# Optimization experiments

Hardware: AMD Instinct MI355X
Metric: run time of the kernel (lower is better)

The kernel has to match this reference:

```python
import jax, jax.numpy as jnp
import numpy as np

N, E, H, C, G = 100000, 400000, 4, 64, 64  # nodes, edges, heads, per-head dim, graphs
NEG_SLOPE = 0.2


def gat_conv(x, src, dst, W, a_src, a_dst, b, num_nodes):
    # PyG GATConv (v1), concat=True, eval mode (no dropout).
    h = (x @ W).reshape(num_nodes, H, C)                      # [N,H,C]
    al_src = (h * a_src).sum(-1)                              # [N,H]
    al_dst = (h * a_dst).sum(-1)                              # [N,H]
    e = jax.nn.leaky_relu(al_src[src] + al_dst[dst], NEG_SLOPE)  # [E',H]
    # segment softmax over incoming edges of each destination node
    m = jax.ops.segment_max(e, dst, num_segments=num_nodes)
    m = jnp.where(jnp.isfinite(m), m, 0.0)
    ex = jnp.exp(e - m[dst])
    s = jax.ops.segment_sum(ex, dst, num_segments=num_nodes)
    alpha = ex / (s[dst] + 1e-16)                             # [E',H]
    msg = h[src] * alpha[..., None]                           # [E',H,C]
    out = jax.ops.segment_sum(msg, dst, num_segments=num_nodes)
    return out.reshape(num_nodes, H * C) + b


def setup_inputs() -> dict:
    key = jax.random.key(0)
    ks = jax.random.split(key, 20)
    p = lambda k, shape: (jax.random.normal(k, shape, dtype=jnp.float32) * 0.05)
    inp = {
        "x": jax.random.normal(ks[0], (N, 2), dtype=jnp.float32),
        "edge_index": jax.random.randint(ks[1], (2, E), 0, N, dtype=jnp.int64),
        "batch": jnp.sort(jax.random.randint(ks[2], (N,), 0, G, dtype=jnp.int64)),
        # layer 1: in=2 -> heads*hidden=256
        "W1": p(ks[3], (2, H * C)), "a1s": p(ks[4], (H, C)), "a1d": p(ks[5], (H, C)), "b1": jnp.zeros((H * C,), jnp.float32),
        # layer 2,3: 256 -> 256
        "W2": p(ks[6], (H * C, H * C)), "a2s": p(ks[7], (H, C)), "a2d": p(ks[8], (H, C)), "b2": jnp.zeros((H * C,), jnp.float32),
        "W3": p(ks[9], (H * C, H * C)), "a3s": p(ks[10], (H, C)), "a3d": p(ks[11], (H, C)), "b3": jnp.zeros((H * C,), jnp.float32),
        # projection MLP 256 -> 512 -> 256
        "Wp1": p(ks[12], (H * C, 512)), "bp1": jnp.zeros((512,), jnp.float32),
        "Wp2": p(ks[13], (512, 256)), "bp2": jnp.zeros((256,), jnp.float32),
    }
    return inp


def reference(x, edge_index, batch, W1, a1s, a1d, b1, W2, a2s, a2d, b2,
              W3, a3s, a3d, b3, Wp1, bp1, Wp2, bp2):
    num_nodes = x.shape[0]
    # add_self_loops=True (PyG GATConv default); same edge set for all layers
    loops = jnp.arange(num_nodes, dtype=edge_index.dtype)
    src = jnp.concatenate([edge_index[0], loops])
    dst = jnp.concatenate([edge_index[1], loops])

    h = jax.nn.elu(gat_conv(x, src, dst, W1, a1s, a1d, b1, num_nodes))
    h = jax.nn.elu(gat_conv(h, src, dst, W2, a2s, a2d, b2, num_nodes))
    h = jax.nn.elu(gat_conv(h, src, dst, W3, a3s, a3d, b3, num_nodes))

    # global_mean_pool over graphs
    sums = jax.ops.segment_sum(h, batch, num_segments=G)            # [G,256]
    cnts = jax.ops.segment_sum(jnp.ones((num_nodes,), h.dtype), batch, num_segments=G)
    pooled = sums / jnp.maximum(cnts, 1.0)[:, None]

    # projection MLP (dropout is identity in eval)
    z = jax.nn.relu(pooled @ Wp1 + bp1)
    return z @ Wp2 + bp2
```

## Files before the change

kernel.cpp:

```cpp
#include <hip/hip_runtime.h>
#include <math.h>

#define HC 256
#define NHEAD 4
#define NEG_SLOPE 0.2f
#define GG 64

typedef unsigned short u16;
typedef unsigned int u32;
typedef __attribute__((ext_vector_type(8))) short short8;
typedef __attribute__((ext_vector_type(4))) float f32x4;

static __device__ inline u16 f2bf_rn(float f) {
  u32 x = __float_as_uint(f);
  u32 r = (x + 0x7fffu + ((x >> 16) & 1u)) >> 16;
  return (u16)r;
}
static __device__ inline float bf2f(u16 u) { return __uint_as_float(((u32)u) << 16); }


__global__ void count_deg_kernel(const int* __restrict__ ei, int E, int Nn, int* __restrict__ deg) {
  int idx = blockIdx.x * 256 + threadIdx.x;
  int Et = E + Nn;
  if (idx >= Et) return;
  int d = (idx < E) ? ei[E + idx] : (idx - E);
  atomicAdd(&deg[d], 1);
}

__global__ void scan_partial_kernel(const int* __restrict__ deg, int Nn,
                                    int* __restrict__ rowptr, int* __restrict__ bsum) {
  __shared__ int s[256];
  int t = threadIdx.x, i = blockIdx.x * 256 + t;
  int v = (i < Nn) ? deg[i] : 0;
  s[t] = v; __syncthreads();
  for (int off = 1; off < 256; off <<= 1) {
    int x = (t >= off) ? s[t - off] : 0; __syncthreads();
    s[t] += x; __syncthreads();
  }
  if (i < Nn) rowptr[i] = s[t] - v;
  if (t == 255) bsum[blockIdx.x] = s[t];
}

__global__ void scan_bsum_kernel(int* __restrict__ bsum, int nb) {
  __shared__ int s[512];
  int t = threadIdx.x;
  int v = (t < nb) ? bsum[t] : 0;
  s[t] = v; __syncthreads();
  for (int off = 1; off < 512; off <<= 1) {
    int x = (t >= off) ? s[t - off] : 0; __syncthreads();
    s[t] += x; __syncthreads();
  }
  if (t < nb) bsum[t] = s[t] - v;
}

__global__ void scan_add_kernel(int* __restrict__ rowptr, const int* __restrict__ bsum,
                                int Nn, int Etot) {
  int i = blockIdx.x * 256 + threadIdx.x;
  if (i < Nn) rowptr[i] += bsum[blockIdx.x];
  if (i == 0) rowptr[Nn] = Etot;
}

__global__ void fill_csr_kernel(const int* __restrict__ ei, int E, int Nn,
                                const int* __restrict__ rowptr, int* __restrict__ cursor,
                                int* __restrict__ col) {
  int idx = blockIdx.x * 256 + threadIdx.x;
  int Et = E + Nn;
  if (idx >= Et) return;
  int s, d;
  if (idx < E) { s = ei[idx]; d = ei[E + idx]; } else { s = d = idx - E; }
  int pos = atomicAdd(&cursor[d], 1);
  col[rowptr[d] + pos] = s;
}


__global__ void convert_w_kernel(const float* __restrict__ W, u16* __restrict__ hi) {
  int idx = blockIdx.x * 256 + threadIdx.x;
  if (idx >= 256 * 256) return;
  int k = idx >> 8, n = idx & 255;
  hi[n * 256 + k] = f2bf_rn(W[idx]);
}


__global__ void prep_va_kernel(const float* __restrict__ W1, const float* __restrict__ a1s,
                               const float* __restrict__ a1d, float* __restrict__ va) {
  int t = threadIdx.x;
  int q = t >> 6, lane = t & 63;
  int c = t;
  float asv = a1s[c], adv = a1d[c];
  float w0 = W1[c], w1 = W1[256 + c];
  float s0 = w0 * asv, s1 = w1 * asv, d0 = w0 * adv, d1 = w1 * adv;
  #pragma unroll
  for (int off = 32; off >= 1; off >>= 1) {
    s0 += __shfl_xor(s0, off, 64); s1 += __shfl_xor(s1, off, 64);
    d0 += __shfl_xor(d0, off, 64); d1 += __shfl_xor(d1, off, 64);
  }
  if (lane == 0) {
    va[q] = s0; va[4 + q] = s1;
    va[8 + q] = d0; va[12 + q] = d1;
  }
}

__global__ void logits1_kernel(const float* __restrict__ x, const float* __restrict__ va,
                               float* __restrict__ als, float* __restrict__ ald, int Nn) {
  int node = blockIdx.x * 256 + threadIdx.x;
  if (node >= Nn) return;
  float2 xv = *(const float2*)&x[(size_t)node * 2];
  float4 vs0 = *(const float4*)&va[0], vs1 = *(const float4*)&va[4];
  float4 vd0 = *(const float4*)&va[8], vd1 = *(const float4*)&va[12];
  float4 s, d;
  s.x = xv.x * vs0.x + xv.y * vs1.x; s.y = xv.x * vs0.y + xv.y * vs1.y;
  s.z = xv.x * vs0.z + xv.y * vs1.z; s.w = xv.x * vs0.w + xv.y * vs1.w;
  d.x = xv.x * vd0.x + xv.y * vd1.x; d.y = xv.x * vd0.y + xv.y * vd1.y;
  d.z = xv.x * vd0.z + xv.y * vd1.z; d.w = xv.x * vd0.w + xv.y * vd1.w;
  *(float4*)&als[node * 4] = s;
  *(float4*)&ald[node * 4] = d;
}

__global__ void sm_gather1_kernel(const float* __restrict__ x,
    const float* __restrict__ als, const float* __restrict__ ald,
    const int* __restrict__ rowptr, const int* __restrict__ col,
    float* __restrict__ xbar, int Nn) {
  int node = blockIdx.x * 256 + threadIdx.x;
  if (node >= Nn) return;
  int rs = rowptr[node], re = rowptr[node + 1];
  float4 ad = *(const float4*)&ald[node * 4];
  float S0 = 0.f, S1 = 0.f, S2 = 0.f, S3 = 0.f;
  float a0 = 0.f, a1 = 0.f, a2 = 0.f, a3 = 0.f, a4 = 0.f, a5 = 0.f, a6 = 0.f, a7 = 0.f;
  for (int i = rs; i < re; ++i) {
    int s = col[i];
    float4 a = *(const float4*)&als[(size_t)s * 4];
    float2 xs = *(const float2*)&x[(size_t)s * 2];
    float e0 = a.x + ad.x; e0 = e0 > 0.f ? e0 : NEG_SLOPE * e0;
    float e1 = a.y + ad.y; e1 = e1 > 0.f ? e1 : NEG_SLOPE * e1;
    float e2 = a.z + ad.z; e2 = e2 > 0.f ? e2 : NEG_SLOPE * e2;
    float e3 = a.w + ad.w; e3 = e3 > 0.f ? e3 : NEG_SLOPE * e3;
    float p0 = __expf(e0), p1 = __expf(e1), p2 = __expf(e2), p3 = __expf(e3);
    S0 += p0; S1 += p1; S2 += p2; S3 += p3;
    a0 += p0 * xs.x; a1 += p0 * xs.y;
    a2 += p1 * xs.x; a3 += p1 * xs.y;
    a4 += p2 * xs.x; a5 += p2 * xs.y;
    a6 += p3 * xs.x; a7 += p3 * xs.y;
  }
  float i0 = 1.f / (S0 + 1e-16f), i1 = 1.f / (S1 + 1e-16f);
  float i2 = 1.f / (S2 + 1e-16f), i3 = 1.f / (S3 + 1e-16f);
  *(float4*)&xbar[(size_t)node * 8]     = make_float4(a0 * i0, a1 * i0, a2 * i1, a3 * i1);
  *(float4*)&xbar[(size_t)node * 8 + 4] = make_float4(a4 * i2, a5 * i2, a6 * i3, a7 * i3);
}

__global__ __launch_bounds__(256) void expand1_kernel(const float* __restrict__ xbar,
    const float* __restrict__ W1, const float* __restrict__ b1,
    u16* __restrict__ out16, int Nn) {
  int node = blockIdx.x * 4 + (threadIdx.x >> 6);
  int lane = threadIdx.x & 63;
  if (node >= Nn) return;
  int hA = lane >> 5;
  float4 xb0 = *(const float4*)&xbar[(size_t)node * 8];
  float4 xb1 = *(const float4*)&xbar[(size_t)node * 8 + 4];
  float xA0 = hA ? xb0.z : xb0.x, xA1 = hA ? xb0.w : xb0.y;
  float xB0 = hA ? xb1.z : xb1.x, xB1 = hA ? xb1.w : xb1.y;
  int cA = 2 * lane, cB = 128 + 2 * lane;
  float2 wA0 = *(const float2*)&W1[cA], wA1 = *(const float2*)&W1[256 + cA];
  float2 wB0 = *(const float2*)&W1[cB], wB1 = *(const float2*)&W1[256 + cB];
  float2 bA = *(const float2*)&b1[cA],  bB = *(const float2*)&b1[cB];
  float o0 = xA0 * wA0.x + xA1 * wA1.x + bA.x;
  float o1 = xA0 * wA0.y + xA1 * wA1.y + bA.y;
  float o2 = xB0 * wB0.x + xB1 * wB1.x + bB.x;
  float o3 = xB0 * wB0.y + xB1 * wB1.y + bB.y;
  o0 = o0 > 0.f ? o0 : (__expf(o0) - 1.0f);
  o1 = o1 > 0.f ? o1 : (__expf(o1) - 1.0f);
  o2 = o2 > 0.f ? o2 : (__expf(o2) - 1.0f);
  o3 = o3 > 0.f ? o3 : (__expf(o3) - 1.0f);
  u32* o32 = (u32*)out16;
  o32[(size_t)node * 128 + lane]      = (u32)f2bf_rn(o0) | ((u32)f2bf_rn(o1) << 16);
  o32[(size_t)node * 128 + 64 + lane] = (u32)f2bf_rn(o2) | ((u32)f2bf_rn(o3) << 16);
}


#define GBM 64
#define GBN 128

__global__ __launch_bounds__(256) void gemm_mfma_kernel(
    const u16* __restrict__ A, const u16* __restrict__ Bt,
    const float* __restrict__ as_, const float* __restrict__ ad_,
    u16* __restrict__ C16, float* __restrict__ als, float* __restrict__ ald, int Mrows) {
  __shared__ __align__(16) u16 smem[24576];
  char* base_ = (char*)smem;
  int bc = blockIdx.x, br = blockIdx.y;
  int tid = threadIdx.x;
  int wid = tid >> 6, lane = tid & 63;
  int wr = wid >> 1, wc = wid & 1;
  int row0 = br * GBM, col0 = bc * GBN;
  int fr = lane & 15, fg = lane >> 4;

  const u16* agp[2];
  int wofA[2];
  #pragma unroll
  for (int p = 0; p < 2; ++p) {
    int row = p * 32 + (tid >> 3), c = tid & 7;
    int gr = row0 + row; if (gr >= Mrows) gr = Mrows - 1;
    agp[p] = A + (size_t)gr * 256 + c * 8;
    wofA[p] = row * 128 + ((c ^ (row & 7)) << 4);
  }
  const u16* bgp[4];
  int wofB[4];
  #pragma unroll
  for (int p = 0; p < 4; ++p) {
    int row = p * 32 + (tid >> 3), c = tid & 7;
    bgp[p] = Bt + (size_t)(col0 + row) * 256 + c * 8;
    wofB[p] = row * 128 + ((c ^ (row & 7)) << 4);
  }
  int rofA[2][2], rofB[2][4];
  #pragma unroll
  for (int ks = 0; ks < 2; ++ks) {
    #pragma unroll
    for (int m = 0; m < 2; ++m) {
      int rl = wr * 32 + m * 16 + fr;
      rofA[ks][m] = rl * 128 + (((ks * 4 + fg) ^ (rl & 7)) << 4);
    }
    #pragma unroll
    for (int n = 0; n < 4; ++n) {
      int cl_ = wc * 64 + n * 16 + fr;
      rofB[ks][n] = cl_ * 128 + (((ks * 4 + fg) ^ (cl_ & 7)) << 4);
    }
  }

  f32x4 acc[2][4];
  #pragma unroll
  for (int m = 0; m < 2; ++m)
    #pragma unroll
    for (int n = 0; n < 4; ++n) acc[m][n] = (f32x4){0.f, 0.f, 0.f, 0.f};

  uint4 va[2], vb[4];
  #pragma unroll
  for (int p = 0; p < 2; ++p) va[p] = *(const uint4*)agp[p];
  #pragma unroll
  for (int p = 0; p < 4; ++p) vb[p] = *(const uint4*)bgp[p];
  #pragma unroll
  for (int p = 0; p < 2; ++p) *(uint4*)(base_ + wofA[p]) = va[p];
  #pragma unroll
  for (int p = 0; p < 4; ++p) *(uint4*)(base_ + 16384 + wofB[p]) = vb[p];
  __syncthreads();

  #pragma unroll
  for (int kt = 0; kt < 4; ++kt) {
    int buf = kt & 1;
    if (kt < 3) {
      #pragma unroll
      for (int p = 0; p < 2; ++p) va[p] = *(const uint4*)(agp[p] + (kt + 1) * 64);
      #pragma unroll
      for (int p = 0; p < 4; ++p) vb[p] = *(const uint4*)(bgp[p] + (kt + 1) * 64);
    }
    #pragma unroll
    for (int ks = 0; ks < 2; ++ks) {
      short8 af[2], bf[4];
      #pragma unroll
      for (int m = 0; m < 2; ++m) af[m] = *(const short8*)(base_ + buf * 8192 + rofA[ks][m]);
      #pragma unroll
      for (int n = 0; n < 4; ++n) bf[n] = *(const short8*)(base_ + 16384 + buf * 16384 + rofB[ks][n]);
      #pragma unroll
      for (int m = 0; m < 2; ++m)
        #pragma unroll
        for (int n = 0; n < 4; ++n)
          acc[m][n] = __builtin_amdgcn_mfma_f32_16x16x32_bf16(af[m], bf[n], acc[m][n], 0, 0, 0);
    }
    if (kt < 3) {
      int nb = buf ^ 1;
      #pragma unroll
      for (int p = 0; p < 2; ++p) *(uint4*)(base_ + nb * 8192 + wofA[p]) = va[p];
      #pragma unroll
      for (int p = 0; p < 4; ++p) *(uint4*)(base_ + 16384 + nb * 16384 + wofB[p]) = vb[p];
      __syncthreads();
    }
  }

  u16* cl = smem;
  __syncthreads();
  #pragma unroll
  for (int m = 0; m < 2; ++m) {
    #pragma unroll
    for (int n = 0; n < 4; ++n) {
      int c = wc * 64 + n * 16 + fr;
      #pragma unroll
      for (int j = 0; j < 4; ++j) {
        int lr = wr * 32 + m * 16 + fg * 4 + j;
        cl[lr * 128 + c] = f2bf_rn(acc[m][n][j]);
      }
    }
  }
  __syncthreads();
  #pragma unroll
  for (int i = 0; i < 4; ++i) {
    int u = i * 256 + tid;
    int lr = u >> 4, ch = u & 15;
    int grow = row0 + lr;
    if (grow < Mrows) {
      uint4 v = *(const uint4*)&cl[lr * 128 + ch * 8];
      *(uint4*)&C16[(size_t)grow * 256 + col0 + ch * 8] = v;
    }
  }

  int head = bc * 2 + wc;
  float asv[4], adv[4];
  #pragma unroll
  for (int n = 0; n < 4; ++n) {
    asv[n] = as_[head * 64 + n * 16 + fr];
    adv[n] = ad_[head * 64 + n * 16 + fr];
  }
  #pragma unroll
  for (int m = 0; m < 2; ++m) {
    #pragma unroll
    for (int j = 0; j < 4; ++j) {
      float ps = 0.f, pd = 0.f;
      #pragma unroll
      for (int n = 0; n < 4; ++n) {
        ps += acc[m][n][j] * asv[n];
        pd += acc[m][n][j] * adv[n];
      }
      #pragma unroll
      for (int off = 1; off < 16; off <<= 1) {
        ps += __shfl_xor(ps, off, 64);
        pd += __shfl_xor(pd, off, 64);
      }
      int grow = row0 + wr * 32 + m * 16 + fg * 4 + j;
      if (fr == 0 && grow < Mrows) {
        als[grow * 4 + head] = ps;
        ald[grow * 4 + head] = pd;
      }
    }
  }
}


__global__ __launch_bounds__(256) void gat_gather_kernel(const u16* __restrict__ h16,
    const float* __restrict__ als, const float* __restrict__ ald,
    const int* __restrict__ rowptr, const int* __restrict__ col,
    const float* __restrict__ bias, u16* __restrict__ out16, int Nn) {
  int node = __builtin_amdgcn_readfirstlane(blockIdx.x * 4 + (threadIdx.x >> 6));
  int lane = threadIdx.x & 63;
  if (node >= Nn) return;
  int rs = rowptr[node], re = rowptr[node + 1];
  int head = lane >> 4;
  float adv = ald[(size_t)node * 4 + head];
  float S = 0.f;
  float a0 = 0.f, a1 = 0.f, a2 = 0.f, a3 = 0.f;
  const uint2* h64 = (const uint2*)h16;
  #pragma unroll 2
  for (int i = rs; i < re; ++i) {
    int s = col[i];
    float e = als[(size_t)s * 4 + head] + adv;
    e = e > 0.f ? e : NEG_SLOPE * e;
    float p = __expf(e);
    S += p;
    uint2 pv = h64[(size_t)s * 64 + lane];
    a0 += p * __uint_as_float(pv.x << 16);
    a1 += p * __uint_as_float(pv.x & 0xffff0000u);
    a2 += p * __uint_as_float(pv.y << 16);
    a3 += p * __uint_as_float(pv.y & 0xffff0000u);
  }
  float iS = 1.f / (S + 1e-16f);
  float4 bv = *(const float4*)&bias[4 * lane];
  float o0 = a0 * iS + bv.x;
  float o1 = a1 * iS + bv.y;
  float o2 = a2 * iS + bv.z;
  float o3 = a3 * iS + bv.w;
  o0 = o0 > 0.f ? o0 : (__expf(o0) - 1.0f);
  o1 = o1 > 0.f ? o1 : (__expf(o1) - 1.0f);
  o2 = o2 > 0.f ? o2 : (__expf(o2) - 1.0f);
  o3 = o3 > 0.f ? o3 : (__expf(o3) - 1.0f);
  uint2 ov;
  ov.x = (u32)f2bf_rn(o0) | ((u32)f2bf_rn(o1) << 16);
  ov.y = (u32)f2bf_rn(o2) | ((u32)f2bf_rn(o3) << 16);
  ((uint2*)out16)[(size_t)node * 64 + lane] = ov;
}


__global__ void bounds_kernel(const int* __restrict__ batch, int Nn, int* __restrict__ bounds) {
  int g = threadIdx.x;
  if (g > GG) return;
  int lo = 0, hi = Nn;
  while (lo < hi) { int mid = (lo + hi) >> 1; if (batch[mid] < g) lo = mid + 1; else hi = mid; }
  bounds[g] = lo;
}

__global__ __launch_bounds__(64) void pool_kernel(const u16* __restrict__ X,
    const int* __restrict__ bounds, float* __restrict__ pooled) {
  int g = blockIdx.x, split = blockIdx.y;
  int lane = threadIdx.x;
  int s = bounds[g], e = bounds[g + 1];
  int cnt = e - s;
  if (cnt <= 0) return;
  int chunk = (cnt + gridDim.y - 1) / gridDim.y;
  int s2 = s + split * chunk, e2 = min(e, s2 + chunk);
  if (s2 >= e2) return;
  int r = lane >> 5, c = lane & 31;
  float acc[8] = {};
  for (int n = s2 + r; n < e2; n += 2) {
    uint4 v = *(const uint4*)&X[(size_t)n * HC + c * 8];
    acc[0] += __uint_as_float(v.x << 16);
    acc[1] += __uint_as_float(v.x & 0xffff0000u);
    acc[2] += __uint_as_float(v.y << 16);
    acc[3] += __uint_as_float(v.y & 0xffff0000u);
    acc[4] += __uint_as_float(v.z << 16);
    acc[5] += __uint_as_float(v.z & 0xffff0000u);
    acc[6] += __uint_as_float(v.w << 16);
    acc[7] += __uint_as_float(v.w & 0xffff0000u);
  }
  #pragma unroll
  for (int j = 0; j < 8; ++j) acc[j] += __shfl_xor(acc[j], 32, 64);
  if (r == 0) {
    #pragma unroll
    for (int j = 0; j < 8; ++j) atomicAdd(&pooled[g * HC + c * 8 + j], acc[j]);
  }
}

__global__ __launch_bounds__(512) void mlp_kernel(const float* __restrict__ pooled,
    const int* __restrict__ bounds, const float* __restrict__ Wp1, const float* __restrict__ bp1,
    const float* __restrict__ Wp2, const float* __restrict__ bp2, float* __restrict__ out) {
  __shared__ float p[256];
  __shared__ float z1[512];
  int g = blockIdx.x, t = threadIdx.x;
  if (t < 256) {
    int cnt = bounds[g + 1] - bounds[g];
    float inv = 1.0f / (float)(cnt > 1 ? cnt : 1);
    p[t] = pooled[g * 256 + t] * inv;
  }
  __syncthreads();
  float a1 = bp1[t];
  for (int k = 0; k < 256; ++k) a1 += p[k] * Wp1[k * 512 + t];
  z1[t] = fmaxf(a1, 0.f);
  __syncthreads();
  if (t < 256) {
    float a2 = bp2[t];
    for (int k = 0; k < 512; ++k) a2 += z1[k] * Wp2[k * 256 + t];
    out[g * 256 + t] = a2;
  }
}


static inline size_t align_up(size_t x, size_t a) { return (x + a - 1) & ~(a - 1); }

extern "C" void kernel_launch(void* const* d_in, const int* in_sizes, int n_in,
                              void* d_out, int out_size, void* d_ws, size_t ws_size,
                              hipStream_t stream) {
  const float* x    = (const float*)d_in[0];
  const int*   ei   = (const int*)d_in[1];
  const int*   batch= (const int*)d_in[2];
  const float* W1   = (const float*)d_in[3];
  const float* a1s  = (const float*)d_in[4];
  const float* a1d  = (const float*)d_in[5];
  const float* b1   = (const float*)d_in[6];
  const float* W2   = (const float*)d_in[7];
  const float* a2s  = (const float*)d_in[8];
  const float* a2d  = (const float*)d_in[9];
  const float* b2   = (const float*)d_in[10];
  const float* W3   = (const float*)d_in[11];
  const float* a3s  = (const float*)d_in[12];
  const float* a3d  = (const float*)d_in[13];
  const float* b3   = (const float*)d_in[14];
  const float* Wp1  = (const float*)d_in[15];
  const float* bp1  = (const float*)d_in[16];
  const float* Wp2  = (const float*)d_in[17];
  const float* bp2  = (const float*)d_in[18];

  const int N = in_sizes[0] / 2;
  const int E = in_sizes[1] / 2;
  const int Et = E + N;

  char* base = (char*)d_ws;
  size_t off = 0;
  auto alloc = [&](size_t bytes) { size_t o = off; off = align_up(off + bytes, 256); return o; };
  u16*   h16    = (u16*)  (base + alloc((size_t)N * HC * 2));
  u16*   xhi    = (u16*)  (base + alloc((size_t)N * HC * 2));
  float* als    = (float*)(base + alloc((size_t)N * 4 * 4));
  float* ald    = (float*)(base + alloc((size_t)N * 4 * 4));
  float* xbar   = (float*)(base + alloc((size_t)N * 8 * 4));
  float* vabuf  = (float*)(base + alloc(16 * 4));
  int*   rowptr = (int*)  (base + alloc((size_t)(N + 1) * 4));
  int*   col    = (int*)  (base + alloc((size_t)Et * 4));
  int*   deg    = (int*)  (base + alloc((size_t)N * 4));
  int*   cursor = (int*)  (base + alloc((size_t)N * 4));
  int*   bsum   = (int*)  (base + alloc(512 * 4));
  int*   bounds = (int*)  (base + alloc((GG + 1) * 4));
  float* pooled = (float*)(base + alloc((size_t)GG * HC * 4));
  (void)ws_size; (void)n_in; (void)out_size;

  u16* W2t = (u16*)deg;
  u16* W3t = (u16*)cursor;

  hipMemsetAsync(deg, 0, (size_t)N * 4, stream);
  hipMemsetAsync(cursor, 0, (size_t)N * 4, stream);
  hipMemsetAsync(pooled, 0, (size_t)GG * HC * 4, stream);

  int ebk = (Et + 255) / 256;
  count_deg_kernel<<<ebk, 256, 0, stream>>>(ei, E, N, deg);
  int NT = (N + 255) / 256;
  scan_partial_kernel<<<NT, 256, 0, stream>>>(deg, N, rowptr, bsum);
  scan_bsum_kernel<<<1, 512, 0, stream>>>(bsum, NT);
  scan_add_kernel<<<NT, 256, 0, stream>>>(rowptr, bsum, N, Et);
  fill_csr_kernel<<<ebk, 256, 0, stream>>>(ei, E, N, rowptr, cursor, col);

  convert_w_kernel<<<256, 256, 0, stream>>>(W2, W2t);
  convert_w_kernel<<<256, 256, 0, stream>>>(W3, W3t);

  dim3 gemm_grid(HC / GBN, (N + GBM - 1) / GBM);
  int nodeblk = (N + 3) / 4;

  prep_va_kernel<<<1, 256, 0, stream>>>(W1, a1s, a1d, vabuf);
  logits1_kernel<<<NT, 256, 0, stream>>>(x, vabuf, als, ald, N);
  sm_gather1_kernel<<<NT, 256, 0, stream>>>(x, als, ald, rowptr, col, xbar, N);
  expand1_kernel<<<nodeblk, 256, 0, stream>>>(xbar, W1, b1, xhi, N);
  gemm_mfma_kernel<<<gemm_grid, 256, 0, stream>>>(xhi, W2t, a2s, a2d, h16, als, ald, N);
  gat_gather_kernel<<<nodeblk, 256, 0, stream>>>(h16, als, ald, rowptr, col, b2, xhi, N);
  gemm_mfma_kernel<<<gemm_grid, 256, 0, stream>>>(xhi, W3t, a3s, a3d, h16, als, ald, N);
  gat_gather_kernel<<<nodeblk, 256, 0, stream>>>(h16, als, ald, rowptr, col, b3, xhi, N);

  bounds_kernel<<<1, 128, 0, stream>>>(batch, N, bounds);
  pool_kernel<<<dim3(GG, 32), 64, 0, stream>>>(xhi, bounds, pooled);
  mlp_kernel<<<GG, 512, 0, stream>>>(pooled, bounds, Wp1, bp1, Wp2, bp2, (float*)d_out);
}
```

Measured before the change: 339.8 us.

## Fuse layer-1 logits into gather, merge prep kernels and memsets

```diff
diff --git a/kernel.cpp b/kernel.cpp
--- a/kernel.cpp
+++ b/kernel.cpp
@@ -73,67 +73,63 @@
 }
 
 
-__global__ void convert_w_kernel(const float* __restrict__ W, u16* __restrict__ hi) {
-  int idx = blockIdx.x * 256 + threadIdx.x;
-  if (idx >= 256 * 256) return;
-  int k = idx >> 8, n = idx & 255;
-  hi[n * 256 + k] = f2bf_rn(W[idx]);
-}
-
-
-__global__ void prep_va_kernel(const float* __restrict__ W1, const float* __restrict__ a1s,
-                               const float* __restrict__ a1d, float* __restrict__ va) {
-  int t = threadIdx.x;
-  int q = t >> 6, lane = t & 63;
-  int c = t;
-  float asv = a1s[c], adv = a1d[c];
-  float w0 = W1[c], w1 = W1[256 + c];
-  float s0 = w0 * asv, s1 = w1 * asv, d0 = w0 * adv, d1 = w1 * adv;
-  #pragma unroll
-  for (int off = 32; off >= 1; off >>= 1) {
-    s0 += __shfl_xor(s0, off, 64); s1 += __shfl_xor(s1, off, 64);
-    d0 += __shfl_xor(d0, off, 64); d1 += __shfl_xor(d1, off, 64);
-  }
-  if (lane == 0) {
-    va[q] = s0; va[4 + q] = s1;
-    va[8 + q] = d0; va[12 + q] = d1;
-  }
-}
-
-__global__ void logits1_kernel(const float* __restrict__ x, const float* __restrict__ va,
-                               float* __restrict__ als, float* __restrict__ ald, int Nn) {
-  int node = blockIdx.x * 256 + threadIdx.x;
+__global__ void prep_misc_kernel(const float* __restrict__ W2, const float* __restrict__ W3,
+                                 u16* __restrict__ W2t, u16* __restrict__ W3t,
+                                 const int* __restrict__ batch, int Nn, int* __restrict__ bounds) {
+  int b = blockIdx.x;
+  if (b < 512) {
+    const float* W = (b < 256) ? W2 : W3;
+    u16* dst = (b < 256) ? W2t : W3t;
+    int idx = (b & 255) * 256 + threadIdx.x;
+    int k = idx >> 8, n = idx & 255;
+    dst[n * 256 + k] = f2bf_rn(W[idx]);
+  } else {
+    int g = threadIdx.x;
+    if (g > GG) return;
+    int lo = 0, hi = Nn;
+    while (lo < hi) { int mid = (lo + hi) >> 1; if (batch[mid] < g) lo = mid + 1; else hi = mid; }
+    bounds[g] = lo;
+  }
+}
+
+
+__global__ __launch_bounds__(256) void l1_fused_kernel(const float* __restrict__ x,
+    const float* __restrict__ W1, const float* __restrict__ a1s, const float* __restrict__ a1d,
+    const int* __restrict__ rowptr, const int* __restrict__ col,
+    float* __restrict__ xbar, int Nn) {
+  __shared__ float va[16];
+  int t = threadIdx.x, q = t >> 6, lane = t & 63;
+  {
+    float asv = a1s[t], adv = a1d[t];
+    float w0 = W1[t], w1 = W1[256 + t];
+    float s0 = w0 * asv, s1 = w1 * asv, d0 = w0 * adv, d1 = w1 * adv;
+    #pragma unroll
+    for (int off = 32; off >= 1; off >>= 1) {
+      s0 += __shfl_xor(s0, off, 64); s1 += __shfl_xor(s1, off, 64);
+      d0 += __shfl_xor(d0, off, 64); d1 += __shfl_xor(d1, off, 64);
+    }
+    if (lane == 0) { va[q] = s0; va[4 + q] = s1; va[8 + q] = d0; va[12 + q] = d1; }
+  }
+  __syncthreads();
+  int node = blockIdx.x * 256 + t;
   if (node >= Nn) return;
-  float2 xv = *(const float2*)&x[(size_t)node * 2];
   float4 vs0 = *(const float4*)&va[0], vs1 = *(const float4*)&va[4];
   float4 vd0 = *(const float4*)&va[8], vd1 = *(const float4*)&va[12];
-  float4 s, d;
-  s.x = xv.x * vs0.x + xv.y * vs1.x; s.y = xv.x * vs0.y + xv.y * vs1.y;
-  s.z = xv.x * vs0.z + xv.y * vs1.z; s.w = xv.x * vs0.w + xv.y * vs1.w;
-  d.x = xv.x * vd0.x + xv.y * vd1.x; d.y = xv.x * vd0.y + xv.y * vd1.y;
-  d.z = xv.x * vd0.z + xv.y * vd1.z; d.w = xv.x * vd0.w + xv.y * vd1.w;
-  *(float4*)&als[node * 4] = s;
-  *(float4*)&ald[node * 4] = d;
-}
-
-__global__ void sm_gather1_kernel(const float* __restrict__ x,
-    const float* __restrict__ als, const float* __restrict__ ald,
-    const int* __restrict__ rowptr, const int* __restrict__ col,
-    float* __restrict__ xbar, int Nn) {
-  int node = blockIdx.x * 256 + threadIdx.x;
-  if (node >= Nn) return;
+  float2 xv = *(const float2*)&x[(size_t)node * 2];
+  float ad0 = xv.x * vd0.x + xv.y * vd1.x;
+  float ad1 = xv.x * vd0.y + xv.y * vd1.y;
+  float ad2 = xv.x * vd0.z + xv.y * vd1.z;
+  float ad3 = xv.x * vd0.w + xv.y * vd1.w;
   int rs = rowptr[node], re = rowptr[node + 1];
-  float4 ad = *(const float4*)&ald[node * 4];
   float S0 = 0.f, S1 = 0.f, S2 = 0.f, S3 = 0.f;
   float a0 = 0.f, a1 = 0.f, a2 = 0.f, a3 = 0.f, a4 = 0.f, a5 = 0.f, a6 = 0.f, a7 = 0.f;
   for (int i = rs; i < re; ++i) {
     int s = col[i];
-    float4 a = *(const float4*)&als[(size_t)s * 4];
     float2 xs = *(const float2*)&x[(size_t)s * 2];
-    float e0 = a.x + ad.x; e0 = e0 > 0.f ? e0 : NEG_SLOPE * e0;
-    float e1 = a.y + ad.y; e1 = e1 > 0.f ? e1 : NEG_SLOPE * e1;
-    float e2 = a.z + ad.z; e2 = e2 > 0.f ? e2 : NEG_SLOPE * e2;
-    float e3 = a.w + ad.w; e3 = e3 > 0.f ? e3 : NEG_SLOPE * e3;
+    float e0 = xs.x * vs0.x + xs.y * vs1.x + ad0; e0 = e0 > 0.f ? e0 : NEG_SLOPE * e0;
+    float e1 = xs.x * vs0.y + xs.y * vs1.y + ad1; e1 = e1 > 0.f ? e1 : NEG_SLOPE * e1;
+    float e2 = xs.x * vs0.z + xs.y * vs1.z + ad2; e2 = e2 > 0.f ? e2 : NEG_SLOPE * e2;
+    float e3 = xs.x * vs0.w + xs.y * vs1.w + ad3; e3 = e3 > 0.f ? e3 : NEG_SLOPE * e3;
     float p0 = __expf(e0), p1 = __expf(e1), p2 = __expf(e2), p3 = __expf(e3);
     S0 += p0; S1 += p1; S2 += p2; S3 += p3;
     a0 += p0 * xs.x; a1 += p0 * xs.y;
@@ -344,7 +340,7 @@
   float S = 0.f;
   float a0 = 0.f, a1 = 0.f, a2 = 0.f, a3 = 0.f;
   const uint2* h64 = (const uint2*)h16;
-  #pragma unroll 2
+  #pragma unroll 4
   for (int i = rs; i < re; ++i) {
     int s = col[i];
     float e = als[(size_t)s * 4 + head] + adv;
@@ -373,14 +369,6 @@
   ((uint2*)out16)[(size_t)node * 64 + lane] = ov;
 }
 
-
-__global__ void bounds_kernel(const int* __restrict__ batch, int Nn, int* __restrict__ bounds) {
-  int g = threadIdx.x;
-  if (g > GG) return;
-  int lo = 0, hi = Nn;
-  while (lo < hi) { int mid = (lo + hi) >> 1; if (batch[mid] < g) lo = mid + 1; else hi = mid; }
-  bounds[g] = lo;
-}
 
 __global__ __launch_bounds__(64) void pool_kernel(const u16* __restrict__ X,
     const int* __restrict__ bounds, float* __restrict__ pooled) {
@@ -474,22 +462,21 @@
   float* als    = (float*)(base + alloc((size_t)N * 4 * 4));
   float* ald    = (float*)(base + alloc((size_t)N * 4 * 4));
   float* xbar   = (float*)(base + alloc((size_t)N * 8 * 4));
-  float* vabuf  = (float*)(base + alloc(16 * 4));
   int*   rowptr = (int*)  (base + alloc((size_t)(N + 1) * 4));
   int*   col    = (int*)  (base + alloc((size_t)Et * 4));
+  size_t zoff0 = off;
   int*   deg    = (int*)  (base + alloc((size_t)N * 4));
   int*   cursor = (int*)  (base + alloc((size_t)N * 4));
+  float* pooled = (float*)(base + alloc((size_t)GG * HC * 4));
+  size_t zbytes = off - zoff0;
   int*   bsum   = (int*)  (base + alloc(512 * 4));
   int*   bounds = (int*)  (base + alloc((GG + 1) * 4));
-  float* pooled = (float*)(base + alloc((size_t)GG * HC * 4));
   (void)ws_size; (void)n_in; (void)out_size;
 
   u16* W2t = (u16*)deg;
   u16* W3t = (u16*)cursor;
 
-  hipMemsetAsync(deg, 0, (size_t)N * 4, stream);
-  hipMemsetAsync(cursor, 0, (size_t)N * 4, stream);
-  hipMemsetAsync(pooled, 0, (size_t)GG * HC * 4, stream);
+  hipMemsetAsync(base + zoff0, 0, zbytes, stream);
 
   int ebk = (Et + 255) / 256;
   count_deg_kernel<<<ebk, 256, 0, stream>>>(ei, E, N, deg);
@@ -499,22 +486,18 @@
   scan_add_kernel<<<NT, 256, 0, stream>>>(rowptr, bsum, N, Et);
   fill_csr_kernel<<<ebk, 256, 0, stream>>>(ei, E, N, rowptr, cursor, col);
 
-  convert_w_kernel<<<256, 256, 0, stream>>>(W2, W2t);
-  convert_w_kernel<<<256, 256, 0, stream>>>(W3, W3t);
+  prep_misc_kernel<<<513, 256, 0, stream>>>(W2, W3, W2t, W3t, batch, N, bounds);
 
   dim3 gemm_grid(HC / GBN, (N + GBM - 1) / GBM);
   int nodeblk = (N + 3) / 4;
 
-  prep_va_kernel<<<1, 256, 0, stream>>>(W1, a1s, a1d, vabuf);
-  logits1_kernel<<<NT, 256, 0, stream>>>(x, vabuf, als, ald, N);
-  sm_gather1_kernel<<<NT, 256, 0, stream>>>(x, als, ald, rowptr, col, xbar, N);
+  l1_fused_kernel<<<NT, 256, 0, stream>>>(x, W1, a1s, a1d, rowptr, col, xbar, N);
   expand1_kernel<<<nodeblk, 256, 0, stream>>>(xbar, W1, b1, xhi, N);
   gemm_mfma_kernel<<<gemm_grid, 256, 0, stream>>>(xhi, W2t, a2s, a2d, h16, als, ald, N);
   gat_gather_kernel<<<nodeblk, 256, 0, stream>>>(h16, als, ald, rowptr, col, b2, xhi, N);
   gemm_mfma_kernel<<<gemm_grid, 256, 0, stream>>>(xhi, W3t, a3s, a3d, h16, als, ald, N);
   gat_gather_kernel<<<nodeblk, 256, 0, stream>>>(h16, als, ald, rowptr, col, b3, xhi, N);
 
-  bounds_kernel<<<1, 128, 0, stream>>>(batch, N, bounds);
   pool_kernel<<<dim3(GG, 32), 64, 0, stream>>>(xhi, bounds, pooled);
   mlp_kernel<<<GG, 512, 0, stream>>>(pooled, bounds, Wp1, bp1, Wp2, bp2, (float*)d_out);
 }
```

New measurement: 321.7 us. 5.3% less time.
